# Kernel tuning notes

Hardware: AMD Instinct MI355X
Metric: run time of the kernel (lower is better)

The kernel has to match this reference:

```python
import jax, jax.numpy as jnp
import numpy as np
from jax import lax

INV_SQRT2 = 1.0 / np.sqrt(2.0).astype(np.float32)
KAPPA = 30.0

# Fixed 3x3 finite-difference filters (torch Conv2d = cross-correlation; lax.conv_general_dilated too)
K_X1 = INV_SQRT2 * jnp.array([[0., 0., 0.], [0., -1., 1.], [0., 0., 0.]], jnp.float32)
K_X2 = INV_SQRT2 * jnp.array([[0., 0., 0.], [-1., 1., 0.], [0., 0., 0.]], jnp.float32)
K_Y1 = INV_SQRT2 * jnp.array([[0., 1., 0.], [0., -1., 0.], [0., 0., 0.]], jnp.float32)
K_Y2 = INV_SQRT2 * jnp.array([[0., 0., 0.], [0., 1., 0.], [0., -1., 0.]], jnp.float32)


def conv3_reflect(x, k):
    # x: [B,1,H,W]; 3x3 single-channel cross-correlation with reflect padding 1
    xp = jnp.pad(x, ((0, 0), (0, 0), (1, 1), (1, 1)), mode='reflect')
    return lax.conv_general_dilated(
        xp, k[None, None].astype(x.dtype), window_strides=(1, 1), padding='VALID',
        dimension_numbers=('NCHW', 'OIHW', 'NCHW'))


def setup_inputs() -> dict:
    key = jax.random.key(0)
    x = jax.random.normal(key, (16, 1, 1024, 1024), dtype=jnp.float32)
    return {"x": x}


def reference(x):
    fy = conv3_reflect(x, K_Y1)
    fx = conv3_reflect(x, K_X1)
    gradf2 = fy * fy + fx * fx
    cI = jnp.exp(-gradf2 / (KAPPA ** 2))  # option == 2
    term = conv3_reflect(fx * cI, K_X2) + conv3_reflect(fy * cI, K_Y2)
    return term
```

## Files before the change

kernel.cpp:

```cpp
#include <hip/hip_runtime.h>
#include <math.h>


#define HH 1024
#define WW 1024

__device__ __forceinline__ void gh_eval(float xc, float xr, float xu,
                                        float& g, float& h) {
    const float c = 0.70710678118654752f;
    float fx = c * (xr - xc);
    float fy = c * (xu - xc);
    float cI = __expf(-(fx * fx + fy * fy) * (1.0f / 900.0f));
    g = fx * cI;
    h = fy * cI;
}

__global__ __launch_bounds__(256)
void pm_kernel(const float* __restrict__ x, float* __restrict__ out) {
    const int H = HH, W = WW;
    const int i = blockIdx.x;
    const int b = blockIdx.y;
    const float* xb = x + (size_t)b * H * W;
    float*       ob = out + (size_t)b * H * W;
    const int j0 = threadIdx.x << 2;

    const int rm = (i >= 1)    ? i - 1 : 1;
    const int rp = (i + 1 < H) ? i + 1 : H - 2;
    const int rq = rp - 1;

    const float4 xrC = *(const float4*)(xb + (size_t)i  * W + j0);
    const float4 xmC = *(const float4*)(xb + (size_t)rm * W + j0);
    const float4 xpC = *(const float4*)(xb + (size_t)rp * W + j0);
    const float4 xqC = *(const float4*)(xb + (size_t)rq * W + j0);

    const int cl = (j0 >= 1)     ? j0 - 1 : 1;
    const int cr = (j0 + 4 < W)  ? j0 + 4 : W - 2;
    const float xr_l = xb[(size_t)i  * W + cl];
    const float xr_r = xb[(size_t)i  * W + cr];
    const float xm_l = xb[(size_t)rm * W + cl];
    const float xp_r = xb[(size_t)rp * W + cr];

    float xr[6] = {xr_l, xrC.x, xrC.y, xrC.z, xrC.w, xr_r};
    float xm[5] = {xm_l, xmC.x, xmC.y, xmC.z, xmC.w};
    float xp[5] = {xpC.x, xpC.y, xpC.z, xpC.w, xp_r};
    float xq[4] = {xqC.x, xqC.y, xqC.z, xqC.w};

    float gC[4], hC[4], hP[4];
#pragma unroll
    for (int k = 0; k < 4; ++k) {
        gh_eval(xr[k + 1], xr[k + 2], xm[k + 1], gC[k], hC[k]);
        float gdum;
        gh_eval(xp[k], xp[k + 1], xq[k], gdum, hP[k]);
    }

    float gL;
    if (j0 == 0) {
        gL = gC[1];
    } else {
        float hdum;
        gh_eval(xr[0], xr[1], xm[0], gL, hdum);
    }

    const float c = 0.70710678118654752f;
    float4 o;
    o.x = c * ((gC[0] - gL)    + (hC[0] - hP[0]));
    o.y = c * ((gC[1] - gC[0]) + (hC[1] - hP[1]));
    o.z = c * ((gC[2] - gC[1]) + (hC[2] - hP[2]));
    o.w = c * ((gC[3] - gC[2]) + (hC[3] - hP[3]));
    *(float4*)(ob + (size_t)i * W + j0) = o;
}

extern "C" void kernel_launch(void* const* d_in, const int* in_sizes, int n_in,
                              void* d_out, int out_size, void* d_ws, size_t ws_size,
                              hipStream_t stream) {
    const float* x = (const float*)d_in[0];
    float* out = (float*)d_out;
    const int total = in_sizes[0];
    const int B = total / (HH * WW);
    dim3 grid(HH, B);
    pm_kernel<<<grid, 256, 0, stream>>>(x, out);
}
```

Baseline: 125.5 us.

## Process eight rows per block with rolling register reuse and nontemporal stores

Each block now computes eight consecutive output rows. It carries the previous row's loaded values and the g/h flux values forward in registers, so each input row is loaded and each flux term evaluated once instead of being recomputed for neighbouring rows. Output is written with nontemporal vector stores to avoid polluting the cache. The grid shrinks by a factor of eight, which lowers parallelism and adds register pressure in exchange for fewer redundant loads and exp evaluations.

```diff
diff --git a/kernel.cpp b/kernel.cpp
--- a/kernel.cpp
+++ b/kernel.cpp
@@ -4,6 +4,9 @@
 
 #define HH 1024
 #define WW 1024
+#define RR 8
+
+typedef float vfloat4 __attribute__((ext_vector_type(4)));
 
 __device__ __forceinline__ void gh_eval(float xc, float xr, float xu,
                                         float& g, float& h) {
@@ -15,59 +18,107 @@
     h = fy * cI;
 }
 
+__device__ __forceinline__ void store_nt4(float* p, float a, float b, float cc, float d) {
+    vfloat4 v = {a, b, cc, d};
+    __builtin_nontemporal_store(v, (vfloat4*)p);
+}
+
 __global__ __launch_bounds__(256)
 void pm_kernel(const float* __restrict__ x, float* __restrict__ out) {
     const int H = HH, W = WW;
-    const int i = blockIdx.x;
-    const int b = blockIdx.y;
+    const int r0 = blockIdx.x * RR;
+    const int b  = blockIdx.y;
     const float* xb = x + (size_t)b * H * W;
     float*       ob = out + (size_t)b * H * W;
     const int j0 = threadIdx.x << 2;
+    const int cl = (j0 >= 1)    ? j0 - 1 : 1;
+    const int cr = (j0 + 4 < W) ? j0 + 4 : W - 2;
+    const float c = 0.70710678118654752f;
 
-    const int rm = (i >= 1)    ? i - 1 : 1;
-    const int rp = (i + 1 < H) ? i + 1 : H - 2;
-    const int rq = rp - 1;
+    float xm[5], xr[6];
+    {
+        const int pm = (r0 >= 1) ? r0 - 1 : 1;
+        const float4 vm = *(const float4*)(xb + (size_t)pm * W + j0);
+        xm[0] = xb[(size_t)pm * W + cl];
+        xm[1] = vm.x; xm[2] = vm.y; xm[3] = vm.z; xm[4] = vm.w;
 
-    const float4 xrC = *(const float4*)(xb + (size_t)i  * W + j0);
-    const float4 xmC = *(const float4*)(xb + (size_t)rm * W + j0);
-    const float4 xpC = *(const float4*)(xb + (size_t)rp * W + j0);
-    const float4 xqC = *(const float4*)(xb + (size_t)rq * W + j0);
-
-    const int cl = (j0 >= 1)     ? j0 - 1 : 1;
-    const int cr = (j0 + 4 < W)  ? j0 + 4 : W - 2;
-    const float xr_l = xb[(size_t)i  * W + cl];
-    const float xr_r = xb[(size_t)i  * W + cr];
-    const float xm_l = xb[(size_t)rm * W + cl];
-    const float xp_r = xb[(size_t)rp * W + cr];
-
-    float xr[6] = {xr_l, xrC.x, xrC.y, xrC.z, xrC.w, xr_r};
-    float xm[5] = {xm_l, xmC.x, xmC.y, xmC.z, xmC.w};
-    float xp[5] = {xpC.x, xpC.y, xpC.z, xpC.w, xp_r};
-    float xq[4] = {xqC.x, xqC.y, xqC.z, xqC.w};
-
-    float gC[4], hC[4], hP[4];
-#pragma unroll
-    for (int k = 0; k < 4; ++k) {
-        gh_eval(xr[k + 1], xr[k + 2], xm[k + 1], gC[k], hC[k]);
-        float gdum;
-        gh_eval(xp[k], xp[k + 1], xq[k], gdum, hP[k]);
+        const float4 vr = *(const float4*)(xb + (size_t)r0 * W + j0);
+        xr[0] = xb[(size_t)r0 * W + cl];
+        xr[1] = vr.x; xr[2] = vr.y; xr[3] = vr.z; xr[4] = vr.w;
+        xr[5] = xb[(size_t)r0 * W + cr];
     }
 
-    float gL;
-    if (j0 == 0) {
-        gL = gC[1];
-    } else {
-        float hdum;
-        gh_eval(xr[0], xr[1], xm[0], gL, hdum);
+    float gw[5], hc[4], hprev[4];
+#pragma unroll
+    for (int t = 0; t < 5; ++t) {
+        float g, h;
+        gh_eval(xr[t], xr[t + 1], xm[t], g, h);
+        gw[t] = g;
+        if (t >= 1) hc[t - 1] = h;
+    }
+    if (j0 == 0) gw[0] = gw[2];
+
+#pragma unroll
+    for (int k = 0; k < RR - 1; ++k) {
+        const int r = r0 + k;
+        float xn[6];
+        {
+            const size_t base = (size_t)(r + 1) * W;
+            const float4 v = *(const float4*)(xb + base + j0);
+            xn[0] = xb[base + cl];
+            xn[1] = v.x; xn[2] = v.y; xn[3] = v.z; xn[4] = v.w;
+            xn[5] = xb[base + cr];
+        }
+        float gw2[5], hn[4];
+#pragma unroll
+        for (int t = 0; t < 5; ++t) {
+            float g, h;
+            gh_eval(xn[t], xn[t + 1], xr[t], g, h);
+            gw2[t] = g;
+            if (t >= 1) hn[t - 1] = h;
+        }
+        if (j0 == 0) gw2[0] = gw2[2];
+
+        store_nt4(ob + (size_t)r * W + j0,
+                  c * ((gw[1] - gw[0]) + (hc[0] - hn[0])),
+                  c * ((gw[2] - gw[1]) + (hc[1] - hn[1])),
+                  c * ((gw[3] - gw[2]) + (hc[2] - hn[2])),
+                  c * ((gw[4] - gw[3]) + (hc[3] - hn[3])));
+
+#pragma unroll
+        for (int t = 0; t < 6; ++t) xr[t] = xn[t];
+#pragma unroll
+        for (int t = 0; t < 5; ++t) gw[t] = gw2[t];
+#pragma unroll
+        for (int t = 0; t < 4; ++t) { hprev[t] = hc[t]; hc[t] = hn[t]; }
     }
 
-    const float c = 0.70710678118654752f;
-    float4 o;
-    o.x = c * ((gC[0] - gL)    + (hC[0] - hP[0]));
-    o.y = c * ((gC[1] - gC[0]) + (hC[1] - hP[1]));
-    o.z = c * ((gC[2] - gC[1]) + (hC[2] - hP[2]));
-    o.w = c * ((gC[3] - gC[2]) + (hC[3] - hP[3]));
-    *(float4*)(ob + (size_t)i * W + j0) = o;
+    {
+        const int rL = r0 + RR - 1;
+        float hP[4];
+        if (rL + 1 < H) {
+            float xn[6];
+            const size_t base = (size_t)(rL + 1) * W;
+            const float4 v = *(const float4*)(xb + base + j0);
+            xn[0] = xb[base + cl];
+            xn[1] = v.x; xn[2] = v.y; xn[3] = v.z; xn[4] = v.w;
+            xn[5] = xb[base + cr];
+#pragma unroll
+            for (int t = 1; t < 5; ++t) {
+                float g, h;
+                gh_eval(xn[t], xn[t + 1], xr[t], g, h);
+                hP[t - 1] = h;
+            }
+        } else {
+            hP[0] = hprev[0]; hP[1] = hprev[1];
+            hP[2] = hprev[2]; hP[3] = hprev[3];
+        }
+        store_nt4(ob + (size_t)rL * W + j0,
+                  c * ((gw[1] - gw[0]) + (hc[0] - hP[0])),
+                  c * ((gw[2] - gw[1]) + (hc[1] - hP[1])),
+                  c * ((gw[3] - gw[2]) + (hc[2] - hP[2])),
+                  c * ((gw[4] - gw[3]) + (hc[3] - hP[3])));
+    }
 }
 
 extern "C" void kernel_launch(void* const* d_in, const int* in_sizes, int n_in,
@@ -77,6 +128,6 @@
     float* out = (float*)d_out;
     const int total = in_sizes[0];
     const int B = total / (HH * WW);
-    dim3 grid(HH, B);
+    dim3 grid(HH / RR, B);
     pm_kernel<<<grid, 256, 0, stream>>>(x, out);
 }
```

After: 111.2 us. 1.13x faster.
